# Performance work log

Measured on AMD Instinct MI355X. Metric: run time of the kernel, lower is better.

The kernel has to match this reference:

```python
import jax, jax.numpy as jnp
import numpy as np

B, N, G, K, V, M = 8, 4096, 128, 16, 64, 64
D, NH, FF = 384, 8, 1536
DH = D // NH


def _ln(x):
    m = jnp.mean(x, -1, keepdims=True)
    v = jnp.mean((x - m) ** 2, -1, keepdims=True)
    return (x - m) * jax.lax.rsqrt(v + 1e-5)


def _attn(q_in, kv_in, w, mask=None):
    # w: [4, D, D] = (Wq, Wk, Wv, Wo)
    Bq, Sq, _ = q_in.shape
    Sk = kv_in.shape[1]
    q = (q_in @ w[0]).reshape(Bq, Sq, NH, DH)
    k = (kv_in @ w[1]).reshape(Bq, Sk, NH, DH)
    v = (kv_in @ w[2]).reshape(Bq, Sk, NH, DH)
    logits = jnp.einsum('bqhd,bkhd->bhqk', q, k) / np.float32(np.sqrt(DH))
    if mask is not None:
        logits = jnp.where(mask[:, None], logits, jnp.float32(-1e9))
    a = jax.nn.softmax(logits, -1)
    return jnp.einsum('bhqk,bkhd->bqhd', a, v).reshape(Bq, Sq, D) @ w[3]


def _ffn(x, w1, w2):
    return jax.nn.relu(x @ w1) @ w2


def _knn(q, ref, k):
    d = (jnp.sum(q * q, -1)[:, :, None] + jnp.sum(ref * ref, -1)[:, None, :]
         - 2.0 * jnp.einsum('bqd,brd->bqr', q, ref))
    return jax.lax.top_k(-d, k)[1]  # [B, Nq, k]


def _fps(pos, m):
    Bc = pos.shape[0]
    d0 = jnp.sum((pos - pos[:, :1]) ** 2, -1)
    def step(mind, _):
        nxt = jnp.argmax(mind, -1)
        p = jnp.take_along_axis(pos, nxt[:, None, None], 1)
        return jnp.minimum(mind, jnp.sum((pos - p) ** 2, -1)), nxt
    _, idxs = jax.lax.scan(step, d0, None, length=m - 1)
    idx = jnp.concatenate([jnp.zeros((Bc, 1), idxs.dtype), idxs.T], 1)
    return jnp.take_along_axis(pos, idx[..., None], 1)  # [B, m, 3]


def _pe(xyz):
    # PositionEmbeddingCoordsSine: 3 -> D, scale=1.0
    cd = D // 3
    dim_t = 10000.0 ** (2.0 * (jnp.arange(cd) // 2) / cd)
    p = xyz[..., None] / dim_t  # [..., 3, cd]
    pe = jnp.stack([jnp.sin(p[..., 0::2]), jnp.cos(p[..., 1::2])], -1)
    return pe.reshape(xyz.shape[:-1] + (D,))


def _gather(x, idx):  # x: [B,S,C], idx: [B,m]
    return jnp.take_along_axis(x, idx[:, :, None], 1)


def _neigh_mask(nidx, S):  # boolean attention mask from knn indices
    Bc, Q, _ = nidx.shape
    return jnp.zeros((Bc, Q, S), bool).at[
        jnp.arange(Bc)[:, None, None], jnp.arange(Q)[None, :, None], nidx].set(True)


def _tokenize(pos, w1, b1, w2, b2, w3, b3, w4, b4):
    centers = _fps(pos, G)
    nidx = _knn(centers, pos, K)
    grouped = pos[jnp.arange(pos.shape[0])[:, None, None], nidx]  # [B,G,K,3]
    rel = grouped - centers[:, :, None, :]
    f = jax.nn.relu(rel @ w1 + b1) @ w2 + b2                       # [B,G,K,256]
    g = jnp.broadcast_to(f.max(2)[:, :, None, :], f.shape)
    tok = (jax.nn.relu(jnp.concatenate([g, f], -1) @ w3 + b3) @ w4 + b4).max(2)
    return tok, centers


def _cross_encoder(src, tgt, src_mask, tgt_mask, cx_attn, cx_ff1, cx_ff2):
    sa, ca = cx_attn[0], cx_attn[1]
    src = src + _attn(_ln(src), _ln(src), sa, src_mask)
    tgt = tgt + _attn(_ln(tgt), _ln(tgt), sa, tgt_mask)
    src2 = src + _attn(_ln(src), _ln(tgt), ca)
    tgt2 = tgt + _attn(_ln(tgt), _ln(src), ca)
    src2 = src2 + _ffn(_ln(src2), cx_ff1, cx_ff2)
    tgt2 = tgt2 + _ffn(_ln(tgt2), cx_ff1, cx_ff2)
    return src2, tgt2


def _dec_blocks(q, q_pos, mem, mem_pos, sa, ca, f1, f2):
    x = q + q_pos
    m = mem + mem_pos
    for l in range(ca.shape[0]):
        if sa is not None:
            x = x + _attn(_ln(x), _ln(x), sa[l])
        x = x + _attn(_ln(x), _ln(m), ca[l])
        x = x + _ffn(_ln(x), f1[l], f2[l])
    return x


def _upsample(pos, centers, feats, w1, b1, w2, b2):
    # PointNet++ feature propagation: 3-NN inverse-distance interpolation + MLP
    d = (jnp.sum(pos * pos, -1)[:, :, None] + jnp.sum(centers * centers, -1)[:, None, :]
         - 2.0 * jnp.einsum('bnd,bgd->bng', pos, centers))
    nd, idx = jax.lax.top_k(-d, 3)
    w = 1.0 / (jnp.maximum(-nd, 0.0) + 1e-8)
    w = w / jnp.sum(w, -1, keepdims=True)
    nb = feats[jnp.arange(pos.shape[0])[:, None, None], idx]  # [B,N,3,D]
    interp = jnp.sum(w[..., None] * nb, 2)
    x = jnp.concatenate([interp, pos], -1)  # concat xyz (points1) -> D+3
    return jax.nn.relu(jax.nn.relu(x @ w1 + b1) @ w2 + b2)


def _smooth_l1(t, p, beta=2.0):
    a = jnp.abs(p - t)
    return jnp.mean(jnp.where(a < beta, 0.5 * a * a / beta, a - 0.5 * beta))


def _forward(pos_src, pos_tgt, tok_w1, tok_b1, tok_w2, tok_b2, tok_w3, tok_b3,
             tok_w4, tok_b4, mask_token, cx_attn, cx_ff1, cx_ff2,
             enc_sa, enc_ca, enc_ff1, enc_ff2, dec_ca, dec_ff1, dec_ff2,
             up_w1, up_b1, up_w2, up_b2,
             vis_idx_src, msk_idx_src, vis_idx_tgt, msk_idx_tgt):
    tokens_src, centers_src = _tokenize(pos_src, tok_w1, tok_b1, tok_w2, tok_b2, tok_w3, tok_b3, tok_w4, tok_b4)
    tokens_tgt, centers_tgt = _tokenize(pos_tgt, tok_w1, tok_b1, tok_w2, tok_b2, tok_w3, tok_b3, tok_w4, tok_b4)
    c_src_pe, c_tgt_pe = _pe(centers_src), _pe(centers_tgt)
    p_src_pe, p_tgt_pe = _pe(pos_src), _pe(pos_tgt)

    vis3_src = _gather(centers_src, vis_idx_src)   # [B,V,3]
    vis3_tgt = _gather(centers_tgt, vis_idx_tgt)
    vtok_src = _gather(tokens_src, vis_idx_src)    # [B,V,D]
    vtok_tgt = _gather(tokens_tgt, vis_idx_tgt)

    m_full_src = _neigh_mask(_knn(centers_src, centers_src, K), G)
    m_full_tgt = _neigh_mask(_knn(centers_tgt, centers_tgt, K), G)
    m_vis_src = _neigh_mask(_knn(vis3_src, vis3_src, K), V)
    m_vis_tgt = _neigh_mask(_knn(vis3_tgt, vis3_tgt, K), V)

    vis_out_src, vis_out_tgt = _cross_encoder(vtok_src, vtok_tgt, m_vis_src, m_vis_tgt, cx_attn, cx_ff1, cx_ff2)
    src_out, tgt_out = _cross_encoder(tokens_src, tokens_tgt, m_full_src, m_full_tgt, cx_attn, cx_ff1, cx_ff2)

    Bc = pos_src.shape[0]
    mt = jnp.broadcast_to(mask_token, (Bc, M, D))
    q_src = jnp.concatenate([mt, vis_out_src], 1)
    qpos_src = jnp.concatenate([_gather(c_src_pe, msk_idx_src), _gather(c_src_pe, vis_idx_src)], 1)
    q_tgt = jnp.concatenate([mt, vis_out_tgt], 1)
    qpos_tgt = jnp.concatenate([_gather(c_tgt_pe, msk_idx_tgt), _gather(c_tgt_pe, vis_idx_tgt)], 1)

    dec_src = _dec_blocks(q_src, qpos_src, tgt_out, c_tgt_pe, enc_sa, enc_ca, enc_ff1, enc_ff2)
    dec_tgt = _dec_blocks(q_tgt, qpos_tgt, src_out, c_src_pe, enc_sa, enc_ca, enc_ff1, enc_ff2)

    t_src = jax.lax.stop_gradient(_gather(src_out, msk_idx_src))
    t_tgt = jax.lax.stop_gradient(_gather(tgt_out, msk_idx_tgt))
    mae = 0.5 * _smooth_l1(t_src, dec_src[:, :M]) + 0.5 * _smooth_l1(t_tgt, dec_tgt[:, :M])

    up_src = _upsample(pos_src, centers_src, src_out, up_w1, up_b1, up_w2, up_b2)
    up_tgt = _upsample(pos_tgt, centers_tgt, tgt_out, up_w1, up_b1, up_w2, up_b2)
    dense_src = _dec_blocks(up_src, p_src_pe, src_out, c_src_pe, None, dec_ca, dec_ff1, dec_ff2)
    dense_tgt = _dec_blocks(up_tgt, p_tgt_pe, tgt_out, c_tgt_pe, None, dec_ca, dec_ff1, dec_ff2)
    return dense_src, dense_tgt, mae


def setup_inputs() -> dict:
    key = jax.random.key(0)
    ks = jax.random.split(key, 32)
    nrm = lambda i, shp: jax.random.normal(ks[i], shp, dtype=jnp.float32) * 0.02
    ps = jax.vmap(lambda k: jax.random.permutation(k, G))(jax.random.split(ks[2], B))
    pt = jax.vmap(lambda k: jax.random.permutation(k, G))(jax.random.split(ks[3], B))
    return {
        'pos_src': jax.random.normal(ks[0], (B, N, 3), dtype=jnp.float32),
        'pos_tgt': jax.random.normal(ks[1], (B, N, 3), dtype=jnp.float32),
        'vis_idx_src': ps[:, :V], 'msk_idx_src': ps[:, V:],
        'vis_idx_tgt': pt[:, :V], 'msk_idx_tgt': pt[:, V:],
        'tok_w1': nrm(4, (3, 128)), 'tok_b1': jnp.zeros((128,), jnp.float32),
        'tok_w2': nrm(5, (128, 256)), 'tok_b2': jnp.zeros((256,), jnp.float32),
        'tok_w3': nrm(6, (512, 512)), 'tok_b3': jnp.zeros((512,), jnp.float32),
        'tok_w4': nrm(7, (512, D)), 'tok_b4': jnp.zeros((D,), jnp.float32),
        'mask_token': nrm(8, (D,)),
        'cx_attn': nrm(9, (2, 4, D, D)), 'cx_ff1': nrm(10, (D, FF)), 'cx_ff2': nrm(11, (FF, D)),
        'enc_sa': nrm(12, (4, 4, D, D)), 'enc_ca': nrm(13, (4, 4, D, D)),
        'enc_ff1': nrm(14, (4, D, FF)), 'enc_ff2': nrm(15, (4, FF, D)),
        'dec_ca': nrm(16, (2, 4, D, D)), 'dec_ff1': nrm(17, (2, D, FF)), 'dec_ff2': nrm(18, (2, FF, D)),
        'up_w1': nrm(19, (D + 3, D)), 'up_b1': jnp.zeros((D,), jnp.float32),
        'up_w2': nrm(20, (D, D)), 'up_b2': jnp.zeros((D,), jnp.float32),
    }


def reference(pos_src, pos_tgt, vis_idx_src, msk_idx_src, vis_idx_tgt, msk_idx_tgt,
              tok_w1, tok_b1, tok_w2, tok_b2, tok_w3, tok_b3, tok_w4, tok_b4,
              mask_token, cx_attn, cx_ff1, cx_ff2, enc_sa, enc_ca, enc_ff1, enc_ff2,
              dec_ca, dec_ff1, dec_ff2, up_w1, up_b1, up_w2, up_b2):
    return _forward(pos_src, pos_tgt, tok_w1, tok_b1, tok_w2, tok_b2, tok_w3, tok_b3,
                    tok_w4, tok_b4, mask_token, cx_attn, cx_ff1, cx_ff2,
                    enc_sa, enc_ca, enc_ff1, enc_ff2, dec_ca, dec_ff1, dec_ff2,
                    up_w1, up_b1, up_w2, up_b2,
                    vis_idx_src, msk_idx_src, vis_idx_tgt, msk_idx_tgt)
```

## Files before the change

### kernel.cpp

```cpp
#include <hip/hip_runtime.h>
#include <hip/hip_bf16.h>
#include <math.h>

using bf16 = __hip_bfloat16;

#define DI static __device__ __forceinline__

constexpr int Bc = 8, Nn = 4096, Gc = 128, Kc = 16, Vc = 64, Mc = 64;
constexpr int Dd = 384, NHh = 8, DHh = 48, FFf = 1536;

typedef __bf16 bf8v __attribute__((ext_vector_type(8)));
typedef float f4v __attribute__((ext_vector_type(4)));

DI float b2f(bf16 h) { return __bfloat162float(h); }
DI __bf16 f2b(float f) { return (__bf16)f; }

DI void gld16(const void* g, void* l) {
    __builtin_amdgcn_global_load_lds((const __attribute__((address_space(1))) void*)g,
                                     (__attribute__((address_space(3))) void*)l, 16, 0, 0);
}

__global__ __launch_bounds__(256) void detect_kernel(const unsigned int* __restrict__ w, int* __restrict__ flag) {
    __shared__ int sh[256];
    int cnt = 0;
// ... 19 lines not shown
                            const int* __restrict__ flag) {
    size_t t = (size_t)blockIdx.x * 256 + threadIdx.x;
    if (t < n) dst[t] = ldf(src, t, flag[0]);
}

__global__ void wtr_kernel(const void* __restrict__ src, __bf16* __restrict__ dst,
                           int K, int N, int Kpad, int cnt, const int* __restrict__ flag) {
    size_t t = (size_t)blockIdx.x * 256 + threadIdx.x;
    size_t total = (size_t)cnt * N * Kpad;
    if (t >= total) return;
    int k = (int)(t % Kpad);
    size_t rem = t / Kpad;
    int n = (int)(rem % N);
    int mat = (int)(rem / N);
    float v = (k < K) ? ldf(src, ((size_t)mat * K + k) * N + n, flag[0]) : 0.f;
    dst[t] = f2b(v);
}

__global__ void zero_kernel(unsigned char* __restrict__ p, size_t n) {
    size_t t = (size_t)blockIdx.x * 256 + threadIdx.x;
    if (t < n) p[t] = 0;
}

__global__ void add_kernel(const float* __restrict__ a, const float* __restrict__ b,
                           float* __restrict__ o, size_t n) {
    size_t t = (size_t)blockIdx.x * 256 + threadIdx.x;
    if (t < n) o[t] = a[t] + b[t];
}

__global__ __launch_bounds__(512) void fps_kernel(const float* __restrict__ pos_a, const float* __restrict__ pos_b,
                                                  float* __restrict__ cent_a, float* __restrict__ cent_b) {
    __shared__ float px[Nn], py[Nn], pz[Nn];
    __shared__ float wv[8];
    __shared__ int wi[8];
    __shared__ int chosen;
    int side = blockIdx.x >> 3, b = blockIdx.x & 7, tid = threadIdx.x;
    const float* pos = side ? pos_b : pos_a;
    float* cent = side ? cent_b : cent_a;
    const float* p = pos + (size_t)b * Nn * 3;
    for (int i = tid; i < Nn; i += 512) { px[i] = p[3*i]; py[i] = p[3*i+1]; pz[i] = p[3*i+2]; }
    __syncthreads();
    float cx = px[0], cy = py[0], cz = pz[0];
    if (tid == 0) { float* c0 = cent + (size_t)b * Gc * 3; c0[0] = cx; c0[1] = cy; c0[2] = cz; }
    float mind[8];
#pragma unroll
    for (int j = 0; j < 8; j++) {
        int i = tid + 512 * j;
        float dx = px[i]-cx, dy = py[i]-cy, dz = pz[i]-cz;
        mind[j] = __fadd_rn(__fadd_rn(__fmul_rn(dx,dx), __fmul_rn(dy,dy)), __fmul_rn(dz,dz));
    }
    for (int s = 1; s < Gc; s++) {
        float bv = -1.f; int bi = 0;
#pragma unroll
        for (int j = 0; j < 8; j++) { int i = tid + 512*j; if (mind[j] > bv) { bv = mind[j]; bi = i; } }
        for (int o = 32; o > 0; o >>= 1) {
            float v2 = __shfl_down(bv, o, 64); int i2 = __shfl_down(bi, o, 64);
            if (v2 > bv || (v2 == bv && i2 < bi)) { bv = v2; bi = i2; }
        }
        if ((tid & 63) == 0) { wv[tid >> 6] = bv; wi[tid >> 6] = bi; }
        __syncthreads();
        if (tid == 0) {
            float fv = wv[0]; int fi = wi[0];
            for (int k = 1; k < 8; k++)
                if (wv[k] > fv || (wv[k] == fv && wi[k] < fi)) { fv = wv[k]; fi = wi[k]; }
            chosen = fi;
            float* cs = cent + ((size_t)b * Gc + s) * 3;
            cs[0] = px[fi]; cs[1] = py[fi]; cs[2] = pz[fi];
        }
        __syncthreads();
        int ci = chosen;
        float qx = px[ci], qy = py[ci], qz = pz[ci];
#pragma unroll
        for (int j = 0; j < 8; j++) {
            int i = tid + 512 * j;
            float dx = px[i]-qx, dy = py[i]-qy, dz = pz[i]-qz;
            float d = __fadd_rn(__fadd_rn(__fmul_rn(dx,dx), __fmul_rn(dy,dy)), __fmul_rn(dz,dz));
            if (d < mind[j]) mind[j] = d;
        }
    }
}

__global__ __launch_bounds__(64) void knn16_kernel(const float* __restrict__ q, const float* __restrict__ r,
                                                   int* __restrict__ nidx, int NQ, int NR) {
    __shared__ float dist[4096];
    int blk = blockIdx.x; int b = blk / NQ, qi = blk % NQ;
    int lane = threadIdx.x;
    const float* qp = q + ((size_t)b * NQ + qi) * 3;
    float qx = qp[0], qy = qp[1], qz = qp[2];
    float qq = __fadd_rn(__fadd_rn(__fmul_rn(qx,qx), __fmul_rn(qy,qy)), __fmul_rn(qz,qz));
    const float* rp = r + (size_t)b * NR * 3;
    for (int i = lane; i < NR; i += 64) {
        float rx = rp[3*i], ry = rp[3*i+1], rz = rp[3*i+2];
        float rr = __fadd_rn(__fadd_rn(__fmul_rn(rx,rx), __fmul_rn(ry,ry)), __fmul_rn(rz,rz));
        float dot = __fadd_rn(__fadd_rn(__fmul_rn(qx,rx), __fmul_rn(qy,ry)), __fmul_rn(qz,rz));
        dist[i] = __fadd_rn(__fadd_rn(qq, rr), -2.f * dot);
    }
    __syncthreads();
    int* out = nidx + ((size_t)b * NQ + qi) * Kc;
    for (int sel = 0; sel < Kc; ++sel) {
        float bv = INFINITY; int bi = 0;
        bool has = false;
// ... 121 lines not shown

__global__ void scatter_mask_kernel(const int* __restrict__ nidx, unsigned char* __restrict__ mask,
                                    int Q, int S, int nb) {
    int t = blockIdx.x * 256 + threadIdx.x;
    if (t >= nb * Q * Kc) return;
    int q = (t / Kc) % Q; int b = t / (Kc * Q);
    mask[((size_t)b * Q + q) * S + nidx[t]] = 1;
}

__global__ void pe_kernel(float* __restrict__ dst, const float* __restrict__ base,
                          const float* __restrict__ xyz, size_t total) {
    size_t t = (size_t)blockIdx.x * 256 + threadIdx.x;
    if (t >= total) return;
    int d = (int)(t % Dd); size_t bs = t / Dd;
    int c = d >> 7;
    int i = d & 127;
    int j = i >> 1;
    float inv = __expf(-0.1439115683121279f * (float)j);
    float val = xyz[bs * 3 + c] * inv;
    float pe = (i & 1) ? __cosf(val) : __sinf(val);
    dst[t] = (base ? base[t] : 0.f) + pe;
}

__global__ __launch_bounds__(256) void ln_kernel(const float* __restrict__ X, __bf16* __restrict__ Y, int R) {
    int lane = threadIdx.x & 63;
    int row = blockIdx.x * 4 + (threadIdx.x >> 6);
    if (row >= R) return;
    const float* x = X + (size_t)row * Dd;
    float v[6]; float s = 0.f;
#pragma unroll
    for (int j = 0; j < 6; j++) { v[j] = x[lane + 64*j]; s += v[j]; }
#pragma unroll
    for (int o = 32; o > 0; o >>= 1) s += __shfl_xor(s, o, 64);
    float m = s * (1.f / Dd);
    float s2 = 0.f;
#pragma unroll
    for (int j = 0; j < 6; j++) { float d = v[j] - m; s2 += d * d; }
#pragma unroll
    for (int o = 32; o > 0; o >>= 1) s2 += __shfl_xor(s2, o, 64);
    float inv = rsqrtf(s2 * (1.f / Dd) + 1e-5f);
    __bf16* y = Y + (size_t)row * Dd;
#pragma unroll
    for (int j = 0; j < 6; j++) y[lane + 64*j] = f2b((v[j] - m) * inv);
}

__global__ __launch_bounds__(256) void gemm_kernel(const __bf16* __restrict__ A, const __bf16* __restrict__ Wt,
                                                   const float* __restrict__ bias,
                                                   const float* __restrict__ res, void* __restrict__ Cv,
                                                   int M, int Ncols, int Kk, int relu, int obf) {
    __shared__ alignas(16) __bf16 As[128*64];
    __shared__ alignas(16) __bf16 Bs[128*64];
    const int tid = threadIdx.x;
    const int row0 = blockIdx.y * 128, col0 = blockIdx.x * 128;
    const int w = tid >> 6, lane = tid & 63, m = lane & 15, q = lane >> 4;
    const int wr = w >> 1, wc = w & 1;
    const int l8 = lane >> 3, l7 = lane & 7;
    const __bf16* apg = A  + (size_t)(row0 + 32*w + l8) * Kk + 8*(l7 ^ l8);
    const __bf16* wpg = Wt + (size_t)(col0 + 32*w + l8) * Kk + 8*(l7 ^ l8);
    const int swz = (m & 7) << 4;
    const char* asb = (const char*)As;
    const char* bsb = (const char*)Bs;

    f4v acc[4][4];
#pragma unroll
    for (int r = 0; r < 4; r++)
#pragma unroll
        for (int n = 0; n < 4; n++) acc[r][n] = (f4v){0.f, 0.f, 0.f, 0.f};

    for (int k0 = 0; k0 < Kk; k0 += 64) {
#pragma unroll
        for (int i = 0; i < 4; i++) {
            gld16(apg + k0 + (size_t)(8*i) * Kk, As + w*2048 + i*512);
            gld16(wpg + k0 + (size_t)(8*i) * Kk, Bs + w*2048 + i*512);
        }
        __syncthreads();
#pragma unroll
        for (int kk = 0; kk < 2; kk++) {
            bf8v bfr[4], afr[4];
#pragma unroll
            for (int n = 0; n < 4; n++)
                bfr[n] = *(const bf8v*)(bsb + (wc*64 + n*16 + m)*128 + ((kk*64 + q*16) ^ swz));
#pragma unroll
            for (int r = 0; r < 4; r++)
                afr[r] = *(const bf8v*)(asb + (wr*64 + r*16 + m)*128 + ((kk*64 + q*16) ^ swz));
#pragma unroll
            for (int r = 0; r < 4; r++)
#pragma unroll
                for (int n = 0; n < 4; n++)
                    acc[r][n] = __builtin_amdgcn_mfma_f32_16x16x32_bf16(afr[r], bfr[n], acc[r][n], 0, 0, 0);
        }
        __syncthreads();
    }
#pragma unroll
    for (int n = 0; n < 4; n++) {
        const int gn = col0 + wc*64 + n*16 + m;
        float bv = bias ? bias[gn] : 0.f;
// ... 249 lines not shown
    const size_t wt_cf1 = walloc(DF);
    const size_t wt_cf2 = walloc(DF);
    const size_t wt_es = walloc((size_t)16 * DD);
    const size_t wt_ec = walloc((size_t)16 * DD);
    const size_t wt_ef1 = walloc((size_t)4 * DF);
    const size_t wt_ef2 = walloc((size_t)4 * DF);
    const size_t wt_dc = walloc((size_t)8 * DD);
    const size_t wt_df1 = walloc((size_t)2 * DF);
    const size_t wt_df2 = walloc((size_t)2 * DF);
    const size_t wt_u1 = walloc((size_t)384 * 448);
    const size_t wt_u2 = walloc((size_t)384 * 384);

    size_t o = 0;
    auto alloc = [&](size_t bytes) -> size_t { size_t r = o; o += (bytes + 255) & ~(size_t)255; return r; };
    const size_t flagO = alloc(256);
    const size_t wtO = alloc(wo * 2);
    const size_t bsO = alloc(2048 * 4);
    const size_t mtokO = alloc(Dd * 4);
    const size_t posfO = alloc(2 * PH * 4);
    const size_t centO = alloc((size_t)16 * Gc * 3 * 4);
    const size_t cpeO  = alloc((size_t)16 * GD * 4);
    const size_t tokO  = alloc((size_t)16 * GD * 4);
    const size_t vtokO = alloc((size_t)16 * Vc * Dd * 4);
    const size_t lnSO = alloc((size_t)16 * GD * 2);
    const size_t lnTO = alloc((size_t)16 * GD * 2);
    const size_t lnmO = alloc((size_t)16 * GD * 2);
    const size_t qbO  = alloc((size_t)16 * GD * 2);
    const size_t qkvbO = alloc((size_t)16 * Gc * 1152 * 4);
    const size_t kvbO  = alloc((size_t)16 * Gc * 768 * 2);
    const size_t kvd0O = alloc((size_t)16 * Gc * 768 * 2);
    const size_t kvd1O = alloc((size_t)16 * Gc * 768 * 2);
    const size_t cxO   = alloc((size_t)16 * GD * 2);
    const size_t decxO = alloc((size_t)16 * GD * 4);
    const size_t membO = alloc((size_t)16 * GD * 4);
    const size_t relbO = alloc((size_t)16 * Gc * Kc * 64 * 2);
    const size_t tbsO = alloc((size_t)Bc * Mc * Dd * 4), tbtO = alloc((size_t)Bc * Mc * Dd * 4);
    const size_t mfullO = alloc((size_t)16 * Gc * Gc);
    const size_t mvisO  = alloc((size_t)16 * Vc * Vc);
    const size_t nidxO = alloc((size_t)16 * Gc * Kc * 4);
    const size_t idx3O = alloc((size_t)16 * Nn * 3 * 4), w3O = alloc((size_t)16 * Nn * 3 * 4);
    const size_t vis3O = alloc((size_t)16 * Vc * 3 * 4);
    const size_t accbO = alloc(64);

    const size_t arenaO = o;
    const size_t arena_bytes = (ws_size > arenaO) ? (ws_size - arenaO) : 0;
    int RP = 128;
    {
        const int cands[10] = {65536, 32768, 16384, 8192, 4096, 2048, 1024, 512, 256, 128};
        for (int ci = 0; ci < 10; ci++) {
            if ((size_t)cands[ci] * 9344 + 8192 <= arena_bytes) { RP = cands[ci]; break; }
        }
    }
    size_t ao = arenaO;
    auto aalloc = [&](size_t bytes) -> size_t { size_t r = ao; ao += (bytes + 255) & ~(size_t)255; return r; };
    const size_t AcbO = aalloc((size_t)RP*448*2);
    const size_t XcO  = aalloc((size_t)RP*384*4);
    const size_t LcO  = aalloc((size_t)RP*384*2);
    const size_t T1O  = aalloc((size_t)RP*384*4);
    const size_t QTO  = aalloc((size_t)RP*384*2);
    const size_t T2O  = aalloc((size_t)RP*384*2);
    const size_t HhO  = aalloc((size_t)RP*1536*2);
    int TC = (int)(arena_bytes / 70200);
    TC &= ~7; if (TC > 2048) TC = 2048; if (TC < 8) TC = 8;
    size_t to = arenaO;
    auto talloc = [&](size_t bytes) -> size_t { size_t r = to; to += (bytes + 255) & ~(size_t)255; return r; };
    const size_t tk1O = talloc((size_t)TC*16*128*2);
    const size_t tk2O = talloc((size_t)TC*16*256*2);
    const size_t tgmO = talloc((size_t)TC*256*2);
    const size_t tcatO = talloc((size_t)TC*16*512*2);
    const size_t thbO = talloc((size_t)TC*16*512*2);
    const size_t t4oO = talloc((size_t)TC*16*384*4);

    auto F = [&](size_t off) -> float* { return (float*)(ws + off); };
    auto I = [&](size_t off) -> int* { return (int*)(ws + off); };
    auto U = [&](size_t off) -> unsigned char* { return (unsigned char*)(ws + off); };
    auto Bf = [&](size_t off) -> __bf16* { return (__bf16*)(ws + off); };
    auto ew = [](size_t n) -> dim3 { return dim3((unsigned)((n + 255) / 256)); };
    const int* flag = I(flagO);
    __bf16* WT = Bf(wtO);
    float* BF = F(bsO);
    const int b_t1 = 0, b_t2 = 128, b_t3 = 384, b_t4 = 896, b_u1 = 1280, b_u2 = 1664;

    auto gemm = [&](const __bf16* A, const __bf16* W, const float* bias, const float* res, void* C,
                    int M, int Ncol, int Kk, int relu, int obf) {
        dim3 g((unsigned)(Ncol / 128), (unsigned)(M / 128));
        gemm_kernel<<<g, 256, 0, stream>>>(A, W, bias, res, C, M, Ncol, Kk, relu, obf);
    };
    auto ln = [&](const float* X, __bf16* Y, int R) {
        ln_kernel<<<dim3((R + 3) / 4), 256, 0, stream>>>(X, Y, R);
    };
    auto attn_old = [&](const float* Qp, const float* Kp, const float* Vp, const unsigned char* mask,
                        __bf16* Op, int Sq, int Sk, int nb, int xorv, int ldq, int ldkv) {
        attn_kernel<<<dim3(Sq, NHh, nb), 64, 0, stream>>>(Qp, Kp, Vp, mask, Op, Sq, Sk, xorv, ldq, ldkv);
    };
    auto attn_mfma = [&](const __bf16* Qp, const __bf16* Kp, const __bf16* Vp, __bf16* Op,
                         int ldq, int ldkv, int ldo, int rpb, int nb, int b0,
                         int bxor, const unsigned char* mask) {
        attn_mfma_kernel<<<dim3(rpb/128, NHh, nb), 256, 0, stream>>>(Qp, Kp, Vp, Op, ldq, ldkv, ldo, rpb, b0, bxor, mask);
    };
    __bf16* ctxb = Bf(cxO);

    auto ffn = [&](float* x, const __bf16* w1t, const __bf16* w2t, int R) {
        ln(x, Bf(lnSO), R);
        for (int r0 = 0; r0 < R; r0 += RP) {
            int rc = (R - r0 < RP) ? (R - r0) : RP;
            gemm(Bf(lnSO) + (size_t)r0*Dd, w1t, nullptr, nullptr, Bf(HhO), rc, FFf, Dd, 1, 1);
            gemm(Bf(HhO), w2t, nullptr, x + (size_t)r0*Dd, x + (size_t)r0*Dd, rc, Dd, FFf, 0, 0);
        }
    };
    auto cross_enc = [&](float* x, const unsigned char* mask, int S) {
        const int R = 16 * S;
        if (S == 128) {
            ln(x, Bf(lnSO), R);
            gemm(Bf(lnSO), WT + wt_cx, nullptr, nullptr, Bf(qkvbO), R, 1152, Dd, 0, 1);
            attn_mfma(Bf(qkvbO), Bf(qkvbO) + 384, Bf(qkvbO) + 768, ctxb, 1152, 1152, Dd, 128, 16, 0, 0, mask);
            gemm(ctxb, WT + wt_cx + 3*DD, nullptr, x, x, R, Dd, Dd, 0, 0);
            ln(x, Bf(lnSO), R);
            gemm(Bf(lnSO), WT + wt_cx + 4*DD, nullptr, nullptr, Bf(qkvbO), R, 1152, Dd, 0, 1);
            attn_mfma(Bf(qkvbO), Bf(qkvbO) + 384, Bf(qkvbO) + 768, ctxb, 1152, 1152, Dd, 128, 16, 0, 8, nullptr);
            gemm(ctxb, WT + wt_cx + 7*DD, nullptr, x, x, R, Dd, Dd, 0, 0);
        } else {
            ln(x, Bf(lnSO), R);
            gemm(Bf(lnSO), WT + wt_cx, nullptr, nullptr, F(qkvbO), R, 1152, Dd, 0, 0);
            attn_old(F(qkvbO), F(qkvbO) + 384, F(qkvbO) + 768, mask, ctxb, S, S, 16, 0, 1152, 1152);
            gemm(ctxb, WT + wt_cx + 3*DD, nullptr, x, x, R, Dd, Dd, 0, 0);
            ln(x, Bf(lnSO), R);
            gemm(Bf(lnSO), WT + wt_cx + 4*DD, nullptr, nullptr, F(qkvbO), R, 1152, Dd, 0, 0);
            attn_old(F(qkvbO), F(qkvbO) + 384, F(qkvbO) + 768, nullptr, ctxb, S, S, 16, 8, 1152, 1152);
            gemm(ctxb, WT + wt_cx + 7*DD, nullptr, x, x, R, Dd, Dd, 0, 0);
        }
        ffn(x, WT + wt_cf1, WT + wt_cf2, R);
    };
    auto decoder4 = [&](float* x) {
        for (int l = 0; l < 4; l++) {
            ln(x, Bf(lnTO), 2048);
            gemm(Bf(lnTO), WT + wt_es + (size_t)l*4*DD, nullptr, nullptr, Bf(qkvbO), 2048, 1152, Dd, 0, 1);
            attn_mfma(Bf(qkvbO), Bf(qkvbO) + 384, Bf(qkvbO) + 768, ctxb, 1152, 1152, Dd, 128, 16, 0, 0, nullptr);
            gemm(ctxb, WT + wt_es + (size_t)l*4*DD + 3*DD, nullptr, x, x, 2048, Dd, Dd, 0, 0);
            ln(x, Bf(lnTO), 2048);
            gemm(Bf(lnTO), WT + wt_ec + (size_t)l*4*DD, nullptr, nullptr, Bf(qbO), 2048, Dd, Dd, 0, 1);
            gemm(Bf(lnmO), WT + wt_ec + (size_t)l*4*DD + DD, nullptr, nullptr, Bf(kvbO), 2048, 768, Dd, 0, 1);
            attn_mfma(Bf(qbO), Bf(kvbO), Bf(kvbO) + 384, ctxb, Dd, 768, Dd, 128, 16, 0, 0, nullptr);
            gemm(ctxb, WT + wt_ec + (size_t)l*4*DD + 3*DD, nullptr, x, x, 2048, Dd, Dd, 0, 0);
            ffn(x, WT + wt_ef1 + (size_t)l*DF, WT + wt_ef2 + (size_t)l*DF, 2048);
        }
    };

    detect_kernel<<<dim3(1), 256, 0, stream>>>((const unsigned int*)pos_src, I(flagO));
    cvtf_kernel<<<ew(PH), 256, 0, stream>>>(pos_src, F(posfO), PH, flag);
    cvtf_kernel<<<ew(PH), 256, 0, stream>>>(pos_tgt, F(posfO) + PH, PH, flag);
    cvtf_kernel<<<dim3(2), 256, 0, stream>>>(mtok, F(mtokO), (size_t)Dd, flag);

    auto wtr = [&](const void* src, size_t dstOff, int K, int N, int Kpad, int cnt) {
        wtr_kernel<<<ew((size_t)cnt * N * Kpad), 256, 0, stream>>>(src, WT + dstOff, K, N, Kpad, cnt, flag);
    };
    wtr(tw1, wt_t1, 3, 128, 64, 1);
    wtr(tw2, wt_t2, 128, 256, 128, 1);
    wtr(tw3, wt_t3, 512, 512, 512, 1);
    wtr(tw4, wt_t4, 512, 384, 512, 1);
    wtr(cxw, wt_cx, 384, 384, 384, 8);
    wtr(cff1, wt_cf1, 384, 1536, 384, 1);
    wtr(cff2, wt_cf2, 1536, 384, 1536, 1);
    wtr(esa, wt_es, 384, 384, 384, 16);
    wtr(eca, wt_ec, 384, 384, 384, 16);
    wtr(eff1, wt_ef1, 384, 1536, 384, 4);
    wtr(eff2, wt_ef2, 1536, 384, 1536, 4);
    wtr(dca, wt_dc, 384, 384, 384, 8);
    wtr(dff1, wt_df1, 384, 1536, 384, 2);
    wtr(dff2, wt_df2, 1536, 384, 1536, 2);
    wtr(uw1, wt_u1, 387, 384, 448, 1);
    wtr(uw2, wt_u2, 384, 384, 384, 1);
    cvtf_kernel<<<ew(128), 256, 0, stream>>>(tb1, BF + b_t1, 128, flag);
    cvtf_kernel<<<ew(256), 256, 0, stream>>>(tb2, BF + b_t2, 256, flag);
    cvtf_kernel<<<ew(512), 256, 0, stream>>>(tb3, BF + b_t3, 512, flag);
    cvtf_kernel<<<ew(384), 256, 0, stream>>>(tb4, BF + b_t4, 384, flag);
    cvtf_kernel<<<ew(384), 256, 0, stream>>>(ub1, BF + b_u1, 384, flag);
    cvtf_kernel<<<ew(384), 256, 0, stream>>>(ub2, BF + b_u2, 384, flag);

    fps_kernel<<<dim3(16), 512, 0, stream>>>(F(posfO), F(posfO) + PH, F(centO), F(centO) + (size_t)Bc*Gc*3);

    knn16_kernel<<<dim3(16*Gc), 64, 0, stream>>>(F(centO), F(posfO), I(nidxO), Gc, Nn);
    rel_kernel<<<ew((size_t)16*Gc*Kc*64), 256, 0, stream>>>(F(posfO), F(centO), I(nidxO), Bf(relbO), 16);
    for (int g0 = 0; g0 < 16*Gc; g0 += TC) {
        const int gc = (16*Gc - g0 < TC) ? (16*Gc - g0) : TC;
        const int RC = gc * Kc;
        gemm(Bf(relbO) + (size_t)g0*Kc*64, WT + wt_t1, BF + b_t1, nullptr, Bf(tk1O), RC, 128, 64, 1, 1);
        gemm(Bf(tk1O), WT + wt_t2, BF + b_t2, nullptr, Bf(tk2O), RC, 256, 128, 0, 1);
        maxk_bf_kernel<<<ew((size_t)gc*256), 256, 0, stream>>>(Bf(tk2O), Bf(tgmO), gc, 256);
        concat_gf_kernel<<<ew((size_t)RC*512), 256, 0, stream>>>(Bf(tgmO), Bf(tk2O), Bf(tcatO), gc);
        gemm(Bf(tcatO), WT + wt_t3, BF + b_t3, nullptr, Bf(thbO), RC, 512, 512, 1, 1);
        gemm(Bf(thbO), WT + wt_t4, BF + b_t4, nullptr, F(t4oO), RC, Dd, 512, 0, 0);
        maxk_f32_kernel<<<ew((size_t)gc*Dd), 256, 0, stream>>>(F(t4oO), F(tokO) + (size_t)g0*Dd, gc, Dd);
    }

    pe_kernel<<<ew((size_t)16*GD), 256, 0, stream>>>(F(cpeO), nullptr, F(centO), (size_t)16*GD);

    gather_rows_kernel<<<ew((size_t)Bc*Vc*Dd), 256, 0, stream>>>(F(tokO), vis_s, F(vtokO), Vc, Dd, Gc);
    gather_rows_kernel<<<ew((size_t)Bc*Vc*Dd), 256, 0, stream>>>(F(tokO) + 8*GD, vis_t, F(vtokO) + (size_t)8*Vc*Dd, Vc, Dd, Gc);
    gather_rows_kernel<<<ew((size_t)Bc*Vc*3), 256, 0, stream>>>(F(centO), vis_s, F(vis3O), Vc, 3, Gc);
    gather_rows_kernel<<<ew((size_t)Bc*Vc*3), 256, 0, stream>>>(F(centO) + (size_t)Bc*Gc*3, vis_t, F(vis3O) + (size_t)8*Vc*3, Vc, 3, Gc);

    zero_kernel<<<ew((size_t)16*Gc*Gc), 256, 0, stream>>>(U(mfullO), (size_t)16*Gc*Gc);
    knn16_kernel<<<dim3(16*Gc), 64, 0, stream>>>(F(centO), F(centO), I(nidxO), Gc, Gc);
    scatter_mask_kernel<<<ew((size_t)16*Gc*Kc), 256, 0, stream>>>(I(nidxO), U(mfullO), Gc, Gc, 16);
    zero_kernel<<<ew((size_t)16*Vc*Vc), 256, 0, stream>>>(U(mvisO), (size_t)16*Vc*Vc);
    knn16_kernel<<<dim3(16*Vc), 64, 0, stream>>>(F(vis3O), F(vis3O), I(nidxO), Vc, Vc);
    scatter_mask_kernel<<<ew((size_t)16*Vc*Kc), 256, 0, stream>>>(I(nidxO), U(mvisO), Vc, Vc, 16);

    cross_enc(F(vtokO), U(mvisO), Vc);
    cross_enc(F(tokO), U(mfullO), Gc);

    dec_init_kernel<<<ew((size_t)Bc*GD), 256, 0, stream>>>(F(mtokO), F(vtokO), F(cpeO), msk_s, vis_s, F(decxO));
    dec_init_kernel<<<ew((size_t)Bc*GD), 256, 0, stream>>>(F(mtokO), F(vtokO) + (size_t)8*Vc*Dd, F(cpeO) + 8*GD, msk_t, vis_t, F(decxO) + 8*GD);
    add_kernel<<<ew((size_t)8*GD), 256, 0, stream>>>(F(tokO) + 8*GD, F(cpeO) + 8*GD, F(membO), (size_t)8*GD);
    add_kernel<<<ew((size_t)8*GD), 256, 0, stream>>>(F(tokO), F(cpeO), F(membO) + 8*GD, (size_t)8*GD);
    ln(F(membO), Bf(lnmO), 2048);
    decoder4(F(decxO));

    zero_kernel<<<dim3(1), 256, 0, stream>>>(U(accbO), 64);
    gather_rows_kernel<<<ew((size_t)Bc*Mc*Dd), 256, 0, stream>>>(F(tokO), msk_s, F(tbsO), Mc, Dd, Gc);
    gather_rows_kernel<<<ew((size_t)Bc*Mc*Dd), 256, 0, stream>>>(F(tokO) + 8*GD, msk_t, F(tbtO), Mc, Dd, Gc);
    sl1_kernel<<<ew((size_t)Bc*Mc*Dd), 256, 0, stream>>>(F(tbsO), F(decxO), F(accbO), 0);
    sl1_kernel<<<ew((size_t)Bc*Mc*Dd), 256, 0, stream>>>(F(tbtO), F(decxO) + 8*GD, F(accbO), 1);

    knn3_kernel<<<dim3(16*Nn), 64, 0, stream>>>(F(posfO), F(centO), I(idx3O), F(w3O));
    add_kernel<<<ew((size_t)16*GD), 256, 0, stream>>>(F(tokO), F(cpeO), F(membO), (size_t)16*GD);
    ln(F(membO), Bf(lnmO), 2048);
    gemm(Bf(lnmO), WT + wt_dc + 0*4*DD + DD, nullptr, nullptr, Bf(kvd0O), 2048, 768, Dd, 0, 1);
    gemm(Bf(lnmO), WT + wt_dc + 1*4*DD + DD, nullptr, nullptr, Bf(kvd1O), 2048, 768, Dd, 0, 1);
    const size_t kvdo[2] = {kvd0O, kvd1O};
    const int RT = 16 * Nn;
    for (int r0 = 0; r0 < RT; r0 += RP) {
        const int rpb = (RP < Nn) ? RP : Nn;
        const int nb = (RP < Nn) ? 1 : RP / Nn;
        const int b0 = r0 / Nn;
        interp_kernel<<<ew((size_t)RP*448), 256, 0, stream>>>(F(tokO), F(posfO), I(idx3O), F(w3O), Bf(AcbO), r0, RP);
        gemm(Bf(AcbO), WT + wt_u1, BF + b_u1, nullptr, Bf(LcO), RP, Dd, 448, 1, 1);
        gemm(Bf(LcO), WT + wt_u2, BF + b_u2, nullptr, F(T1O), RP, Dd, Dd, 1, 0);
        pe_kernel<<<ew((size_t)RP*Dd), 256, 0, stream>>>(F(XcO), F(T1O), F(posfO) + (size_t)r0*3, (size_t)RP*Dd);
        for (int l = 0; l < 2; l++) {
            ln(F(XcO), Bf(LcO), RP);
            gemm(Bf(LcO), WT + wt_dc + (size_t)l*4*DD, nullptr, nullptr, Bf(QTO), RP, Dd, Dd, 0, 1);
            attn_mfma(Bf(QTO), Bf(kvdo[l]), Bf(kvdo[l]) + 384, Bf(T2O), Dd, 768, Dd, rpb, nb, b0, 0, nullptr);
            gemm(Bf(T2O), WT + wt_dc + (size_t)l*4*DD + 3*DD, nullptr, F(XcO), F(XcO), RP, Dd, Dd, 0, 0);
            ln(F(XcO), Bf(LcO), RP);
            gemm(Bf(LcO), WT + wt_df1 + (size_t)l*DF, nullptr, nullptr, Bf(HhO), RP, FFf, Dd, 1, 1);
            if (l == 1)
                gemm(Bf(HhO), WT + wt_df2 + DF, nullptr, F(XcO), out + (size_t)r0*Dd, RP, Dd, FFf, 0, 0);
            else
                gemm(Bf(HhO), WT + wt_df2, nullptr, F(XcO), F(XcO), RP, Dd, FFf, 0, 0);
        }
    }

    mae_finalize_kernel<<<dim3(1), 1, 0, stream>>>(F(accbO), out + (size_t)2*Bc*Nn*Dd);
}
```

Measured before the change: 3.372 ms.

## Fuse layernorm into GEMM A-load, fuse PE into GEMM epilogue, shrink FPS block

Adds a gemmln kernel that computes per-row mean and inverse std, then normalises fp32 activations while staging them into LDS as bf16. This replaces the separate ln kernel and its bf16 intermediate before every QKV/Q/FF1 GEMM. The positional-embedding add moves into the up-projection GEMM epilogue, and add+ln pairs become a single ln2 kernel, freeing buffers and lowering the per-row arena cost. FPS now runs 256 threads with 16 points each and writes centers from LDS at the end. The fused GEMM recomputes row statistics in every column block and loads A with plain register loads instead of async LDS loads, which may hurt wide-N GEMMs like FF1.

```diff
diff --git a/kernel.cpp b/kernel.cpp
--- a/kernel.cpp
+++ b/kernel.cpp
@@ -65,37 +65,32 @@
     if (t < n) p[t] = 0;
 }
 
-__global__ void add_kernel(const float* __restrict__ a, const float* __restrict__ b,
-                           float* __restrict__ o, size_t n) {
-    size_t t = (size_t)blockIdx.x * 256 + threadIdx.x;
-    if (t < n) o[t] = a[t] + b[t];
-}
-
-__global__ __launch_bounds__(512) void fps_kernel(const float* __restrict__ pos_a, const float* __restrict__ pos_b,
+__global__ __launch_bounds__(256) void fps_kernel(const float* __restrict__ pos_a, const float* __restrict__ pos_b,
                                                   float* __restrict__ cent_a, float* __restrict__ cent_b) {
     __shared__ float px[Nn], py[Nn], pz[Nn];
-    __shared__ float wv[8];
-    __shared__ int wi[8];
+    __shared__ float csx[Gc], csy[Gc], csz[Gc];
+    __shared__ float wv[4];
+    __shared__ int wi[4];
     __shared__ int chosen;
     int side = blockIdx.x >> 3, b = blockIdx.x & 7, tid = threadIdx.x;
     const float* pos = side ? pos_b : pos_a;
-    float* cent = side ? cent_b : cent_a;
+    float* cent = (side ? cent_b : cent_a) + (size_t)b * Gc * 3;
     const float* p = pos + (size_t)b * Nn * 3;
-    for (int i = tid; i < Nn; i += 512) { px[i] = p[3*i]; py[i] = p[3*i+1]; pz[i] = p[3*i+2]; }
+    for (int i = tid; i < Nn; i += 256) { px[i] = p[3*i]; py[i] = p[3*i+1]; pz[i] = p[3*i+2]; }
     __syncthreads();
     float cx = px[0], cy = py[0], cz = pz[0];
-    if (tid == 0) { float* c0 = cent + (size_t)b * Gc * 3; c0[0] = cx; c0[1] = cy; c0[2] = cz; }
-    float mind[8];
-#pragma unroll
-    for (int j = 0; j < 8; j++) {
-        int i = tid + 512 * j;
+    if (tid == 0) { csx[0] = cx; csy[0] = cy; csz[0] = cz; }
+    float mind[16];
+#pragma unroll
+    for (int j = 0; j < 16; j++) {
+        int i = tid + 256 * j;
         float dx = px[i]-cx, dy = py[i]-cy, dz = pz[i]-cz;
         mind[j] = __fadd_rn(__fadd_rn(__fmul_rn(dx,dx), __fmul_rn(dy,dy)), __fmul_rn(dz,dz));
     }
     for (int s = 1; s < Gc; s++) {
         float bv = -1.f; int bi = 0;
 #pragma unroll
-        for (int j = 0; j < 8; j++) { int i = tid + 512*j; if (mind[j] > bv) { bv = mind[j]; bi = i; } }
+        for (int j = 0; j < 16; j++) { int i = tid + 256*j; if (mind[j] > bv) { bv = mind[j]; bi = i; } }
         for (int o = 32; o > 0; o >>= 1) {
             float v2 = __shfl_down(bv, o, 64); int i2 = __shfl_down(bi, o, 64);
             if (v2 > bv || (v2 == bv && i2 < bi)) { bv = v2; bi = i2; }
@@ -104,22 +99,25 @@
         __syncthreads();
         if (tid == 0) {
             float fv = wv[0]; int fi = wi[0];
-            for (int k = 1; k < 8; k++)
+            for (int k = 1; k < 4; k++)
                 if (wv[k] > fv || (wv[k] == fv && wi[k] < fi)) { fv = wv[k]; fi = wi[k]; }
             chosen = fi;
-            float* cs = cent + ((size_t)b * Gc + s) * 3;
-            cs[0] = px[fi]; cs[1] = py[fi]; cs[2] = pz[fi];
+            csx[s] = px[fi]; csy[s] = py[fi]; csz[s] = pz[fi];
         }
         __syncthreads();
         int ci = chosen;
         float qx = px[ci], qy = py[ci], qz = pz[ci];
 #pragma unroll
-        for (int j = 0; j < 8; j++) {
-            int i = tid + 512 * j;
+        for (int j = 0; j < 16; j++) {
+            int i = tid + 256 * j;
             float dx = px[i]-qx, dy = py[i]-qy, dz = pz[i]-qz;
             float d = __fadd_rn(__fadd_rn(__fmul_rn(dx,dx), __fmul_rn(dy,dy)), __fmul_rn(dz,dz));
             if (d < mind[j]) mind[j] = d;
         }
+    }
+    __syncthreads();
+    for (int i = tid; i < Gc; i += 256) {
+        cent[3*i] = csx[i]; cent[3*i+1] = csy[i]; cent[3*i+2] = csz[i];
     }
 }
 
@@ -287,14 +285,16 @@
     dst[t] = (base ? base[t] : 0.f) + pe;
 }
 
-__global__ __launch_bounds__(256) void ln_kernel(const float* __restrict__ X, __bf16* __restrict__ Y, int R) {
+__global__ __launch_bounds__(256) void ln2_kernel(const float* __restrict__ A, const float* __restrict__ B,
+                                                  __bf16* __restrict__ Y, int R) {
     int lane = threadIdx.x & 63;
     int row = blockIdx.x * 4 + (threadIdx.x >> 6);
     if (row >= R) return;
-    const float* x = X + (size_t)row * Dd;
+    const float* a = A + (size_t)row * Dd;
+    const float* b = B + (size_t)row * Dd;
     float v[6]; float s = 0.f;
 #pragma unroll
-    for (int j = 0; j < 6; j++) { v[j] = x[lane + 64*j]; s += v[j]; }
+    for (int j = 0; j < 6; j++) { v[j] = a[lane + 64*j] + b[lane + 64*j]; s += v[j]; }
 #pragma unroll
     for (int o = 32; o > 0; o >>= 1) s += __shfl_xor(s, o, 64);
     float m = s * (1.f / Dd);
@@ -312,7 +312,8 @@
 __global__ __launch_bounds__(256) void gemm_kernel(const __bf16* __restrict__ A, const __bf16* __restrict__ Wt,
                                                    const float* __restrict__ bias,
                                                    const float* __restrict__ res, void* __restrict__ Cv,
-                                                   int M, int Ncols, int Kk, int relu, int obf) {
+                                                   int M, int Ncols, int Kk, int relu, int obf,
+                                                   const float* __restrict__ pepos) {
     __shared__ alignas(16) __bf16 As[128*64];
     __shared__ alignas(16) __bf16 Bs[128*64];
     const int tid = threadIdx.x;
@@ -337,6 +338,110 @@
         for (int i = 0; i < 4; i++) {
             gld16(apg + k0 + (size_t)(8*i) * Kk, As + w*2048 + i*512);
             gld16(wpg + k0 + (size_t)(8*i) * Kk, Bs + w*2048 + i*512);
+        }
+        __syncthreads();
+#pragma unroll
+        for (int kk = 0; kk < 2; kk++) {
+            bf8v bfr[4], afr[4];
+#pragma unroll
+            for (int n = 0; n < 4; n++)
+                bfr[n] = *(const bf8v*)(bsb + (wc*64 + n*16 + m)*128 + ((kk*64 + q*16) ^ swz));
+#pragma unroll
+            for (int r = 0; r < 4; r++)
+                afr[r] = *(const bf8v*)(asb + (wr*64 + r*16 + m)*128 + ((kk*64 + q*16) ^ swz));
+#pragma unroll
+            for (int r = 0; r < 4; r++)
+#pragma unroll
+                for (int n = 0; n < 4; n++)
+                    acc[r][n] = __builtin_amdgcn_mfma_f32_16x16x32_bf16(afr[r], bfr[n], acc[r][n], 0, 0, 0);
+        }
+        __syncthreads();
+    }
+#pragma unroll
+    for (int n = 0; n < 4; n++) {
+        const int gn = col0 + wc*64 + n*16 + m;
+        float bv = bias ? bias[gn] : 0.f;
+        const int pi = gn & 127, pc = gn >> 7, pj = pi >> 1;
+        const float pinv = pepos ? __expf(-0.1439115683121279f * (float)pj) : 0.f;
+#pragma unroll
+        for (int r = 0; r < 4; r++) {
+#pragma unroll
+            for (int j = 0; j < 4; j++) {
+                int gm = row0 + wr*64 + r*16 + q*4 + j;
+                float v = acc[r][n][j] + bv;
+                if (relu) v = fmaxf(v, 0.f);
+                if (pepos) {
+                    float val = pepos[(size_t)gm*3 + pc] * pinv;
+                    v += (pi & 1) ? __cosf(val) : __sinf(val);
+                }
+                if (res) v += res[(size_t)gm * Ncols + gn];
+                if (obf) ((__bf16*)Cv)[(size_t)gm * Ncols + gn] = f2b(v);
+                else     ((float*)Cv)[(size_t)gm * Ncols + gn] = v;
+            }
+        }
+    }
+}
+
+__global__ __launch_bounds__(256) void gemmln_kernel(const float* __restrict__ Af, const __bf16* __restrict__ Wt,
+                                                     const float* __restrict__ bias,
+                                                     const float* __restrict__ res, void* __restrict__ Cv,
+                                                     int M, int Ncols, int Kk, int relu, int obf) {
+    __shared__ alignas(16) __bf16 As[128*64];
+    __shared__ alignas(16) __bf16 Bs[128*64];
+    __shared__ float mu[128], iv[128];
+    const int tid = threadIdx.x;
+    const int row0 = blockIdx.y * 128, col0 = blockIdx.x * 128;
+    const int w = tid >> 6, lane = tid & 63, m = lane & 15, q = lane >> 4;
+    const int wr = w >> 1, wc = w & 1;
+    const int l8 = lane >> 3, l7 = lane & 7;
+    const __bf16* wpg = Wt + (size_t)(col0 + 32*w + l8) * Kk + 8*(l7 ^ l8);
+    const int swz = (m & 7) << 4;
+    const char* asb = (const char*)As;
+    const char* bsb = (const char*)Bs;
+
+    for (int r = 0; r < 32; r++) {
+        int row = w*32 + r;
+        const float* x = Af + (size_t)(row0 + row) * Kk;
+        float v[6]; float s = 0.f;
+#pragma unroll
+        for (int j = 0; j < 6; j++) { v[j] = x[lane + 64*j]; s += v[j]; }
+#pragma unroll
+        for (int o = 32; o > 0; o >>= 1) s += __shfl_xor(s, o, 64);
+        float mean = s * (1.f / Dd);
+        float s2 = 0.f;
+#pragma unroll
+        for (int j = 0; j < 6; j++) { float d = v[j] - mean; s2 += d * d; }
+#pragma unroll
+        for (int o = 32; o > 0; o >>= 1) s2 += __shfl_xor(s2, o, 64);
+        if (lane == 0) { mu[row] = mean; iv[row] = rsqrtf(s2 * (1.f / Dd) + 1e-5f); }
+    }
+    __syncthreads();
+    const int srow = tid >> 1, s0 = (tid & 1) * 4;
+    const float* arow = Af + (size_t)(row0 + srow) * Kk;
+    const float mean_ = mu[srow], inv_ = iv[srow];
+
+    f4v acc[4][4];
+#pragma unroll
+    for (int r = 0; r < 4; r++)
+#pragma unroll
+        for (int n = 0; n < 4; n++) acc[r][n] = (f4v){0.f, 0.f, 0.f, 0.f};
+
+    for (int k0 = 0; k0 < Kk; k0 += 64) {
+#pragma unroll
+        for (int i = 0; i < 4; i++)
+            gld16(wpg + k0 + (size_t)(8*i) * Kk, Bs + w*2048 + i*512);
+#pragma unroll
+        for (int si = 0; si < 4; si++) {
+            int s = s0 + ((si + srow) & 3);
+            int srck = k0 + 8*(s ^ (srow & 7));
+            float4 f0 = *reinterpret_cast<const float4*>(arow + srck);
+            float4 f1 = *reinterpret_cast<const float4*>(arow + srck + 4);
+            union { __bf16 h[8]; uint4 u; } t;
+            t.h[0] = f2b((f0.x - mean_) * inv_); t.h[1] = f2b((f0.y - mean_) * inv_);
+            t.h[2] = f2b((f0.z - mean_) * inv_); t.h[3] = f2b((f0.w - mean_) * inv_);
+            t.h[4] = f2b((f1.x - mean_) * inv_); t.h[5] = f2b((f1.y - mean_) * inv_);
+            t.h[6] = f2b((f1.z - mean_) * inv_); t.h[7] = f2b((f1.w - mean_) * inv_);
+            *reinterpret_cast<uint4*>(&As[srow*64 + s*8]) = t.u;
         }
         __syncthreads();
 #pragma unroll
@@ -632,8 +737,6 @@
     const size_t cpeO  = alloc((size_t)16 * GD * 4);
     const size_t tokO  = alloc((size_t)16 * GD * 4);
     const size_t vtokO = alloc((size_t)16 * Vc * Dd * 4);
-    const size_t lnSO = alloc((size_t)16 * GD * 2);
-    const size_t lnTO = alloc((size_t)16 * GD * 2);
     const size_t lnmO = alloc((size_t)16 * GD * 2);
     const size_t qbO  = alloc((size_t)16 * GD * 2);
     const size_t qkvbO = alloc((size_t)16 * Gc * 1152 * 4);
@@ -642,7 +745,6 @@
     const size_t kvd1O = alloc((size_t)16 * Gc * 768 * 2);
     const size_t cxO   = alloc((size_t)16 * GD * 2);
     const size_t decxO = alloc((size_t)16 * GD * 4);
-    const size_t membO = alloc((size_t)16 * GD * 4);
     const size_t relbO = alloc((size_t)16 * Gc * Kc * 64 * 2);
     const size_t tbsO = alloc((size_t)Bc * Mc * Dd * 4), tbtO = alloc((size_t)Bc * Mc * Dd * 4);
     const size_t mfullO = alloc((size_t)16 * Gc * Gc);
@@ -658,7 +760,7 @@
     {
         const int cands[10] = {65536, 32768, 16384, 8192, 4096, 2048, 1024, 512, 256, 128};
         for (int ci = 0; ci < 10; ci++) {
-            if ((size_t)cands[ci] * 9344 + 8192 <= arena_bytes) { RP = cands[ci]; break; }
+            if ((size_t)cands[ci] * 7808 + 8192 <= arena_bytes) { RP = cands[ci]; break; }
         }
     }
     size_t ao = arenaO;
@@ -666,7 +768,6 @@
     const size_t AcbO = aalloc((size_t)RP*448*2);
     const size_t XcO  = aalloc((size_t)RP*384*4);
     const size_t LcO  = aalloc((size_t)RP*384*2);
-    const size_t T1O  = aalloc((size_t)RP*384*4);
     const size_t QTO  = aalloc((size_t)RP*384*2);
     const size_t T2O  = aalloc((size_t)RP*384*2);
     const size_t HhO  = aalloc((size_t)RP*1536*2);
@@ -694,10 +795,20 @@
     auto gemm = [&](const __bf16* A, const __bf16* W, const float* bias, const float* res, void* C,
                     int M, int Ncol, int Kk, int relu, int obf) {
         dim3 g((unsigned)(Ncol / 128), (unsigned)(M / 128));
-        gemm_kernel<<<g, 256, 0, stream>>>(A, W, bias, res, C, M, Ncol, Kk, relu, obf);
+        gemm_kernel<<<g, 256, 0, stream>>>(A, W, bias, res, C, M, Ncol, Kk, relu, obf, nullptr);
     };
-    auto ln = [&](const float* X, __bf16* Y, int R) {
-        ln_kernel<<<dim3((R + 3) / 4), 256, 0, stream>>>(X, Y, R);
+    auto gemm_pe = [&](const __bf16* A, const __bf16* W, const float* bias, void* C,
+                       int M, int Ncol, int Kk, const float* pepos) {
+        dim3 g((unsigned)(Ncol / 128), (unsigned)(M / 128));
+        gemm_kernel<<<g, 256, 0, stream>>>(A, W, bias, nullptr, C, M, Ncol, Kk, 1, 0, pepos);
+    };
+    auto gemmln = [&](const float* A, const __bf16* W, const float* res, void* C,
+                      int M, int Ncol, int relu, int obf) {
+        dim3 g((unsigned)(Ncol / 128), (unsigned)(M / 128));
+        gemmln_kernel<<<g, 256, 0, stream>>>(A, W, nullptr, res, C, M, Ncol, Dd, relu, obf);
+    };
+    auto ln2 = [&](const float* A, const float* B, __bf16* Y, int R) {
+        ln2_kernel<<<dim3((R + 3) / 4), 256, 0, stream>>>(A, B, Y, R);
     };
     auto attn_old = [&](const float* Qp, const float* Kp, const float* Vp, const unsigned char* mask,
                         __bf16* Op, int Sq, int Sk, int nb, int xorv, int ldq, int ldkv) {
@@ -711,31 +822,26 @@
     __bf16* ctxb = Bf(cxO);
 
     auto ffn = [&](float* x, const __bf16* w1t, const __bf16* w2t, int R) {
-        ln(x, Bf(lnSO), R);
         for (int r0 = 0; r0 < R; r0 += RP) {
             int rc = (R - r0 < RP) ? (R - r0) : RP;
-            gemm(Bf(lnSO) + (size_t)r0*Dd, w1t, nullptr, nullptr, Bf(HhO), rc, FFf, Dd, 1, 1);
+            gemmln(x + (size_t)r0*Dd, w1t, nullptr, Bf(HhO), rc, FFf, 1, 1);
             gemm(Bf(HhO), w2t, nullptr, x + (size_t)r0*Dd, x + (size_t)r0*Dd, rc, Dd, FFf, 0, 0);
         }
     };
     auto cross_enc = [&](float* x, const unsigned char* mask, int S) {
         const int R = 16 * S;
         if (S == 128) {
-            ln(x, Bf(lnSO), R);
-            gemm(Bf(lnSO), WT + wt_cx, nullptr, nullptr, Bf(qkvbO), R, 1152, Dd, 0, 1);
+            gemmln(x, WT + wt_cx, nullptr, Bf(qkvbO), R, 1152, 0, 1);
             attn_mfma(Bf(qkvbO), Bf(qkvbO) + 384, Bf(qkvbO) + 768, ctxb, 1152, 1152, Dd, 128, 16, 0, 0, mask);
             gemm(ctxb, WT + wt_cx + 3*DD, nullptr, x, x, R, Dd, Dd, 0, 0);
-            ln(x, Bf(lnSO), R);
-            gemm(Bf(lnSO), WT + wt_cx + 4*DD, nullptr, nullptr, Bf(qkvbO), R, 1152, Dd, 0, 1);
+            gemmln(x, WT + wt_cx + 4*DD, nullptr, Bf(qkvbO), R, 1152, 0, 1);
             attn_mfma(Bf(qkvbO), Bf(qkvbO) + 384, Bf(qkvbO) + 768, ctxb, 1152, 1152, Dd, 128, 16, 0, 8, nullptr);
             gemm(ctxb, WT + wt_cx + 7*DD, nullptr, x, x, R, Dd, Dd, 0, 0);
         } else {
-            ln(x, Bf(lnSO), R);
-            gemm(Bf(lnSO), WT + wt_cx, nullptr, nullptr, F(qkvbO), R, 1152, Dd, 0, 0);
+            gemmln(x, WT + wt_cx, nullptr, F(qkvbO), R, 1152, 0, 0);
             attn_old(F(qkvbO), F(qkvbO) + 384, F(qkvbO) + 768, mask, ctxb, S, S, 16, 0, 1152, 1152);
             gemm(ctxb, WT + wt_cx + 3*DD, nullptr, x, x, R, Dd, Dd, 0, 0);
-            ln(x, Bf(lnSO), R);
-            gemm(Bf(lnSO), WT + wt_cx + 4*DD, nullptr, nullptr, F(qkvbO), R, 1152, Dd, 0, 0);
+            gemmln(x, WT + wt_cx + 4*DD, nullptr, F(qkvbO), R, 1152, 0, 0);
             attn_old(F(qkvbO), F(qkvbO) + 384, F(qkvbO) + 768, nullptr, ctxb, S, S, 16, 8, 1152, 1152);
             gemm(ctxb, WT + wt_cx + 7*DD, nullptr, x, x, R, Dd, Dd, 0, 0);
         }
@@ -743,12 +849,10 @@
     };
     auto decoder4 = [&](float* x) {
         for (int l = 0; l < 4; l++) {
-            ln(x, Bf(lnTO), 2048);
-            gemm(Bf(lnTO), WT + wt_es + (size_t)l*4*DD, nullptr, nullptr, Bf(qkvbO), 2048, 1152, Dd, 0, 1);
+            gemmln(x, WT + wt_es + (size_t)l*4*DD, nullptr, Bf(qkvbO), 2048, 1152, 0, 1);
             attn_mfma(Bf(qkvbO), Bf(qkvbO) + 384, Bf(qkvbO) + 768, ctxb, 1152, 1152, Dd, 128, 16, 0, 0, nullptr);
             gemm(ctxb, WT + wt_es + (size_t)l*4*DD + 3*DD, nullptr, x, x, 2048, Dd, Dd, 0, 0);
-            ln(x, Bf(lnTO), 2048);
-            gemm(Bf(lnTO), WT + wt_ec + (size_t)l*4*DD, nullptr, nullptr, Bf(qbO), 2048, Dd, Dd, 0, 1);
+            gemmln(x, WT + wt_ec + (size_t)l*4*DD, nullptr, Bf(qbO), 2048, Dd, 0, 1);
             gemm(Bf(lnmO), WT + wt_ec + (size_t)l*4*DD + DD, nullptr, nullptr, Bf(kvbO), 2048, 768, Dd, 0, 1);
             attn_mfma(Bf(qbO), Bf(kvbO), Bf(kvbO) + 384, ctxb, Dd, 768, Dd, 128, 16, 0, 0, nullptr);
             gemm(ctxb, WT + wt_ec + (size_t)l*4*DD + 3*DD, nullptr, x, x, 2048, Dd, Dd, 0, 0);
@@ -787,7 +891,7 @@
     cvtf_kernel<<<ew(384), 256, 0, stream>>>(ub1, BF + b_u1, 384, flag);
     cvtf_kernel<<<ew(384), 256, 0, stream>>>(ub2, BF + b_u2, 384, flag);
 
-    fps_kernel<<<dim3(16), 512, 0, stream>>>(F(posfO), F(posfO) + PH, F(centO), F(centO) + (size_t)Bc*Gc*3);
+    fps_kernel<<<dim3(16), 256, 0, stream>>>(F(posfO), F(posfO) + PH, F(centO), F(centO) + (size_t)Bc*Gc*3);
 
     knn16_kernel<<<dim3(16*Gc), 64, 0, stream>>>(F(centO), F(posfO), I(nidxO), Gc, Nn);
     rel_kernel<<<ew((size_t)16*Gc*Kc*64), 256, 0, stream>>>(F(posfO), F(centO), I(nidxO), Bf(relbO), 16);
@@ -822,9 +926,8 @@
 
     dec_init_kernel<<<ew((size_t)Bc*GD), 256, 0, stream>>>(F(mtokO), F(vtokO), F(cpeO), msk_s, vis_s, F(decxO));
     dec_init_kernel<<<ew((size_t)Bc*GD), 256, 0, stream>>>(F(mtokO), F(vtokO) + (size_t)8*Vc*Dd, F(cpeO) + 8*GD, msk_t, vis_t, F(decxO) + 8*GD);
-    add_kernel<<<ew((size_t)8*GD), 256, 0, stream>>>(F(tokO) + 8*GD, F(cpeO) + 8*GD, F(membO), (size_t)8*GD);
-    add_kernel<<<ew((size_t)8*GD), 256, 0, stream>>>(F(tokO), F(cpeO), F(membO) + 8*GD, (size_t)8*GD);
-    ln(F(membO), Bf(lnmO), 2048);
+    ln2(F(tokO) + 8*GD, F(cpeO) + 8*GD, Bf(lnmO), 1024);
+    ln2(F(tokO), F(cpeO), Bf(lnmO) + (size_t)1024*Dd, 1024);
     decoder4(F(decxO));
 
     zero_kernel<<<dim3(1), 256, 0, stream>>>(U(accbO), 64);
@@ -834,8 +937,7 @@
     sl1_kernel<<<ew((size_t)Bc*Mc*Dd), 256, 0, stream>>>(F(tbtO), F(decxO) + 8*GD, F(accbO), 1);
 
     knn3_kernel<<<dim3(16*Nn), 64, 0, stream>>>(F(posfO), F(centO), I(idx3O), F(w3O));
-    add_kernel<<<ew((size_t)16*GD), 256, 0, stream>>>(F(tokO), F(cpeO), F(membO), (size_t)16*GD);
-    ln(F(membO), Bf(lnmO), 2048);
+    ln2(F(tokO), F(cpeO), Bf(lnmO), 2048);
     gemm(Bf(lnmO), WT + wt_dc + 0*4*DD + DD, nullptr, nullptr, Bf(kvd0O), 2048, 768, Dd, 0, 1);
     gemm(Bf(lnmO), WT + wt_dc + 1*4*DD + DD, nullptr, nullptr, Bf(kvd1O), 2048, 768, Dd, 0, 1);
     const size_t kvdo[2] = {kvd0O, kvd1O};
@@ -846,15 +948,12 @@
         const int b0 = r0 / Nn;
         interp_kernel<<<ew((size_t)RP*448), 256, 0, stream>>>(F(tokO), F(posfO), I(idx3O), F(w3O), Bf(AcbO), r0, RP);
         gemm(Bf(AcbO), WT + wt_u1, BF + b_u1, nullptr, Bf(LcO), RP, Dd, 448, 1, 1);
-        gemm(Bf(LcO), WT + wt_u2, BF + b_u2, nullptr, F(T1O), RP, Dd, Dd, 1, 0);
-        pe_kernel<<<ew((size_t)RP*Dd), 256, 0, stream>>>(F(XcO), F(T1O), F(posfO) + (size_t)r0*3, (size_t)RP*Dd);
+        gemm_pe(Bf(LcO), WT + wt_u2, BF + b_u2, F(XcO), RP, Dd, Dd, F(posfO) + (size_t)r0*3);
         for (int l = 0; l < 2; l++) {
-            ln(F(XcO), Bf(LcO), RP);
-            gemm(Bf(LcO), WT + wt_dc + (size_t)l*4*DD, nullptr, nullptr, Bf(QTO), RP, Dd, Dd, 0, 1);
+            gemmln(F(XcO), WT + wt_dc + (size_t)l*4*DD, nullptr, Bf(QTO), RP, Dd, 0, 1);
             attn_mfma(Bf(QTO), Bf(kvdo[l]), Bf(kvdo[l]) + 384, Bf(T2O), Dd, 768, Dd, rpb, nb, b0, 0, nullptr);
             gemm(Bf(T2O), WT + wt_dc + (size_t)l*4*DD + 3*DD, nullptr, F(XcO), F(XcO), RP, Dd, Dd, 0, 0);
-            ln(F(XcO), Bf(LcO), RP);
-            gemm(Bf(LcO), WT + wt_df1 + (size_t)l*DF, nullptr, nullptr, Bf(HhO), RP, FFf, Dd, 1, 1);
+            gemmln(F(XcO), WT + wt_df1 + (size_t)l*DF, nullptr, Bf(HhO), RP, FFf, 1, 1);
             if (l == 1)
                 gemm(Bf(HhO), WT + wt_df2 + DF, nullptr, F(XcO), out + (size_t)r0*Dd, RP, Dd, FFf, 0, 0);
             else
```

After: 4.810 ms. 42.7% more time.
